# Optimization experiments

Measured on AMD Instinct MI355X. Metric: run time of the kernel, lower is better.

The kernel has to match this reference:

```python
import jax, jax.numpy as jnp
import numpy as np


def _shift_kernels():
    # [4,1,3,3] OIHW: left, right, up, down shift-difference kernels (as in torch module)
    kl = [[0, 0, 0], [-1, 1, 0], [0, 0, 0]]
    kr = [[0, 0, 0], [0, 1, -1], [0, 0, 0]]
    ku = [[0, -1, 0], [0, 1, 0], [0, 0, 0]]
    kd = [[0, 0, 0], [0, 1, 0], [0, -1, 0]]
    return jnp.asarray(np.stack([kl, kr, ku, kd])[:, None], dtype=jnp.float32)


def _avgpool4(x):
    # x: [B,1,H,W] -> [B,1,H//4,W//4], non-overlapping 4x4 mean (nn.AvgPool2d(4))
    b, c, h, w = x.shape
    return x.reshape(b, c, h // 4, 4, w // 4, 4).mean(axis=(3, 5))


def setup_inputs() -> dict:
    key = jax.random.key(0)
    k1, k2 = jax.random.split(key)
    org = jax.random.uniform(k1, (32, 3, 512, 512), dtype=jnp.float32)
    enhance = jax.random.uniform(k2, (32, 3, 512, 512), dtype=jnp.float32)
    return {"org": org, "enhance": enhance}


def reference(org, enhance):
    org_pool = _avgpool4(jnp.mean(org, axis=1, keepdims=True))
    enh_pool = _avgpool4(jnp.mean(enhance, axis=1, keepdims=True))
    # conv is linear, so D_org_k - D_enh_k == conv(org_pool - enh_pool, k).
    diff = org_pool - enh_pool  # [B,1,h,w]
    d = jax.lax.conv_general_dilated(
        diff, _shift_kernels(), window_strides=(1, 1),
        padding=((1, 1), (1, 1)),
        dimension_numbers=("NCHW", "OIHW", "NCHW"))  # [B,4,h,w]
    # torch: mean(D_left + D_right + D_up + D_down) over [B,1,h,w]
    return jnp.mean(jnp.sum(d * d, axis=1))
```

## Files before the change

kernel.cpp:

```cpp
#include <hip/hip_runtime.h>

#define NB 32
#define NC 3
#define NH 512
#define NW 512
#define PH 128
#define PW 128
#define NPOOL  (NB * PH * PW)
#define NPLANE (NB * NC)
#define PLANE_ELEMS (PH * PW)
#define NITEMS (NPLANE * PLANE_ELEMS)
#define NBLK_A 1024
#define ITEMS_A 6
#define STRIDE_A (NBLK_A * 256)
#define NBLK_RED (NPOOL / 256)

typedef float vf4 __attribute__((ext_vector_type(4)));

__device__ __forceinline__ int item_base(int item) {
    return ((item >> 14) << 16) + (((item >> 7) & 127) << 9) + (item & 127);
}

__global__ __launch_bounds__(256) void stageA_pool_kernel(
    const vf4* __restrict__ o4, const vf4* __restrict__ e4,
    float* __restrict__ partial)
{
    int item = blockIdx.x * 256 + threadIdx.x;

    int base = item_base(item);
    vf4 oc0 = __builtin_nontemporal_load(o4 + base);
    vf4 oc1 = __builtin_nontemporal_load(o4 + base + 128);
    vf4 oc2 = __builtin_nontemporal_load(o4 + base + 256);
    vf4 oc3 = __builtin_nontemporal_load(o4 + base + 384);
    vf4 ec0 = __builtin_nontemporal_load(e4 + base);
    vf4 ec1 = __builtin_nontemporal_load(e4 + base + 128);
    vf4 ec2 = __builtin_nontemporal_load(e4 + base + 256);
    vf4 ec3 = __builtin_nontemporal_load(e4 + base + 384);

#pragma unroll
    for (int it = 0; it < ITEMS_A; ++it) {
        vf4 on0, on1, on2, on3, en0, en1, en2, en3;
        if (it < ITEMS_A - 1) {
            int nbase = item_base(item + STRIDE_A);
            on0 = __builtin_nontemporal_load(o4 + nbase);
            on1 = __builtin_nontemporal_load(o4 + nbase + 128);
            on2 = __builtin_nontemporal_load(o4 + nbase + 256);
            on3 = __builtin_nontemporal_load(o4 + nbase + 384);
            en0 = __builtin_nontemporal_load(e4 + nbase);
            en1 = __builtin_nontemporal_load(e4 + nbase + 128);
            en2 = __builtin_nontemporal_load(e4 + nbase + 256);
            en3 = __builtin_nontemporal_load(e4 + nbase + 384);
        }

        vf4 d = ((oc0 - ec0) + (oc1 - ec1)) + ((oc2 - ec2) + (oc3 - ec3));
        float v = (d.x + d.y) + (d.z + d.w);
        partial[item] = v * (1.0f / 48.0f);

        if (it < ITEMS_A - 1) {
            oc0 = on0; oc1 = on1; oc2 = on2; oc3 = on3;
            ec0 = en0; ec1 = en1; ec2 = en2; ec3 = en3;
            item += STRIDE_A;
        }
    }
}

__global__ __launch_bounds__(256) void spa_reduce_kernel(
    const float* __restrict__ partial, float* __restrict__ partials_out)
{
    int idx = blockIdx.x * blockDim.x + threadIdx.x;
    int pw = idx & (PW - 1);
    int ph = (idx >> 7) & (PH - 1);
    int b  = idx >> 14;

    const float* p0 = partial + (b * 3 + 0) * PLANE_ELEMS;
    const float* p1 = partial + (b * 3 + 1) * PLANE_ELEMS;
    const float* p2 = partial + (b * 3 + 2) * PLANE_ELEMS;

    #define POOLED(y, x) (p0[(y) * PW + (x)] + p1[(y) * PW + (x)] + p2[(y) * PW + (x)])
    float c = POOLED(ph, pw);
    float l = (pw > 0)      ? POOLED(ph, pw - 1) : 0.f;
    float r = (pw < PW - 1) ? POOLED(ph, pw + 1) : 0.f;
    float u = (ph > 0)      ? POOLED(ph - 1, pw) : 0.f;
    float d = (ph < PH - 1) ? POOLED(ph + 1, pw) : 0.f;
    #undef POOLED

    float dl = c - l, dr = c - r, du = c - u, dd = c - d;
    float s = (dl * dl + dr * dr) + (du * du + dd * dd);

#pragma unroll
    for (int off = 32; off > 0; off >>= 1)
        s += __shfl_down(s, off, 64);

    __shared__ float smem[4];
    int lane = threadIdx.x & 63;
    int wid  = threadIdx.x >> 6;
    if (lane == 0) smem[wid] = s;
    __syncthreads();
    if (threadIdx.x == 0)
        partials_out[blockIdx.x] = (smem[0] + smem[1]) + (smem[2] + smem[3]);
}

__global__ __launch_bounds__(256) void final_reduce_kernel(
    const float* __restrict__ partials, float* __restrict__ out)
{
    float s = 0.f;
#pragma unroll
    for (int i = 0; i < NBLK_RED / 256; ++i)
        s += partials[i * 256 + threadIdx.x];

#pragma unroll
    for (int off = 32; off > 0; off >>= 1)
        s += __shfl_down(s, off, 64);

    __shared__ float smem[4];
    int lane = threadIdx.x & 63;
    int wid  = threadIdx.x >> 6;
    if (lane == 0) smem[wid] = s;
    __syncthreads();
    if (threadIdx.x == 0)
        out[0] = ((smem[0] + smem[1]) + (smem[2] + smem[3])) * (1.0f / (float)NPOOL);
}

extern "C" void kernel_launch(void* const* d_in, const int* in_sizes, int n_in,
                              void* d_out, int out_size, void* d_ws, size_t ws_size,
                              hipStream_t stream) {
    const vf4* o4 = (const vf4*)d_in[0];
    const vf4* e4 = (const vf4*)d_in[1];
    float* out = (float*)d_out;
    float* partial      = (float*)d_ws;
    float* blockpartial = (float*)d_ws + NITEMS;

    stageA_pool_kernel<<<NBLK_A, 256, 0, stream>>>(o4, e4, partial);
    spa_reduce_kernel<<<NBLK_RED, 256, 0, stream>>>(partial, blockpartial);
    final_reduce_kernel<<<1, 256, 0, stream>>>(blockpartial, out);
}
```

Before: 197.6 us.

## Fuse channel sum into pooling, replace final reduce kernel with atomics

The pooling kernel now reads all three channels per output pixel (12 vector loads each of org and enhance) and writes a single pooled plane per batch, instead of per-channel partials. This cuts the intermediate buffer to a third and simplifies the stencil kernel's reads. The final reduction kernel is removed in favour of one atomicAdd per block into the output, which the first kernel zeroes. This saves a launch but makes float summation order nondeterministic, and drops the software pipelining of the old loop in favour of more loads in flight per thread.

```diff
diff --git a/kernel.cpp b/kernel.cpp
--- a/kernel.cpp
+++ b/kernel.cpp
@@ -1,90 +1,59 @@
 #include <hip/hip_runtime.h>
 
 #define NB 32
-#define NC 3
-#define NH 512
-#define NW 512
 #define PH 128
 #define PW 128
 #define NPOOL  (NB * PH * PW)
-#define NPLANE (NB * NC)
-#define PLANE_ELEMS (PH * PW)
-#define NITEMS (NPLANE * PLANE_ELEMS)
-#define NBLK_A 1024
-#define ITEMS_A 6
-#define STRIDE_A (NBLK_A * 256)
-#define NBLK_RED (NPOOL / 256)
+#define NBLK   (NPOOL / 256)
+#define INV48  (1.0f / 48.0f)
 
 typedef float vf4 __attribute__((ext_vector_type(4)));
 
-__device__ __forceinline__ int item_base(int item) {
-    return ((item >> 14) << 16) + (((item >> 7) & 127) << 9) + (item & 127);
-}
+__global__ __launch_bounds__(256) void pool_fused_kernel(
+    const vf4* __restrict__ o4, const vf4* __restrict__ e4,
+    float* __restrict__ pooled, float* __restrict__ out)
+{
+    if (blockIdx.x == 0 && threadIdx.x == 0) out[0] = 0.f;
 
-__global__ __launch_bounds__(256) void stageA_pool_kernel(
-    const vf4* __restrict__ o4, const vf4* __restrict__ e4,
-    float* __restrict__ partial)
-{
-    int item = blockIdx.x * 256 + threadIdx.x;
+    int idx = blockIdx.x * 256 + threadIdx.x;
+    int x = idx & (PW - 1);
+    int y = (idx >> 7) & (PH - 1);
+    int b = idx >> 14;
 
-    int base = item_base(item);
-    vf4 oc0 = __builtin_nontemporal_load(o4 + base);
-    vf4 oc1 = __builtin_nontemporal_load(o4 + base + 128);
-    vf4 oc2 = __builtin_nontemporal_load(o4 + base + 256);
-    vf4 oc3 = __builtin_nontemporal_load(o4 + base + 384);
-    vf4 ec0 = __builtin_nontemporal_load(e4 + base);
-    vf4 ec1 = __builtin_nontemporal_load(e4 + base + 128);
-    vf4 ec2 = __builtin_nontemporal_load(e4 + base + 256);
-    vf4 ec3 = __builtin_nontemporal_load(e4 + base + 384);
+    int rbase = ((b * 3) * 512 + (y << 2)) * 128 + x;
 
+    vf4 ov[12], ev[12];
 #pragma unroll
-    for (int it = 0; it < ITEMS_A; ++it) {
-        vf4 on0, on1, on2, on3, en0, en1, en2, en3;
-        if (it < ITEMS_A - 1) {
-            int nbase = item_base(item + STRIDE_A);
-            on0 = __builtin_nontemporal_load(o4 + nbase);
-            on1 = __builtin_nontemporal_load(o4 + nbase + 128);
-            on2 = __builtin_nontemporal_load(o4 + nbase + 256);
-            on3 = __builtin_nontemporal_load(o4 + nbase + 384);
-            en0 = __builtin_nontemporal_load(e4 + nbase);
-            en1 = __builtin_nontemporal_load(e4 + nbase + 128);
-            en2 = __builtin_nontemporal_load(e4 + nbase + 256);
-            en3 = __builtin_nontemporal_load(e4 + nbase + 384);
-        }
+    for (int i = 0; i < 12; ++i) {
+        int c = i >> 2, dy = i & 3;
+        int a = rbase + (c * 512 + dy) * 128;
+        ov[i] = __builtin_nontemporal_load(o4 + a);
+        ev[i] = __builtin_nontemporal_load(e4 + a);
+    }
 
-        vf4 d = ((oc0 - ec0) + (oc1 - ec1)) + ((oc2 - ec2) + (oc3 - ec3));
-        float v = (d.x + d.y) + (d.z + d.w);
-        partial[item] = v * (1.0f / 48.0f);
+    vf4 d = {0.f, 0.f, 0.f, 0.f};
+#pragma unroll
+    for (int i = 0; i < 12; ++i)
+        d += ov[i] - ev[i];
 
-        if (it < ITEMS_A - 1) {
-            oc0 = on0; oc1 = on1; oc2 = on2; oc3 = on3;
-            ec0 = en0; ec1 = en1; ec2 = en2; ec3 = en3;
-            item += STRIDE_A;
-        }
-    }
+    pooled[idx] = ((d.x + d.y) + (d.z + d.w)) * INV48;
 }
 
 __global__ __launch_bounds__(256) void spa_reduce_kernel(
-    const float* __restrict__ partial, float* __restrict__ partials_out)
+    const float* __restrict__ pooled, float* __restrict__ out)
 {
-    int idx = blockIdx.x * blockDim.x + threadIdx.x;
-    int pw = idx & (PW - 1);
-    int ph = (idx >> 7) & (PH - 1);
-    int b  = idx >> 14;
+    int idx = blockIdx.x * 256 + threadIdx.x;
+    int x = idx & (PW - 1);
+    int y = (idx >> 7) & (PH - 1);
+    const float* p = pooled + (idx >> 14) * (PH * PW);
 
-    const float* p0 = partial + (b * 3 + 0) * PLANE_ELEMS;
-    const float* p1 = partial + (b * 3 + 1) * PLANE_ELEMS;
-    const float* p2 = partial + (b * 3 + 2) * PLANE_ELEMS;
+    float c  = p[y * PW + x];
+    float l  = (x > 0)      ? p[y * PW + x - 1] : 0.f;
+    float r  = (x < PW - 1) ? p[y * PW + x + 1] : 0.f;
+    float u  = (y > 0)      ? p[(y - 1) * PW + x] : 0.f;
+    float dn = (y < PH - 1) ? p[(y + 1) * PW + x] : 0.f;
 
-    #define POOLED(y, x) (p0[(y) * PW + (x)] + p1[(y) * PW + (x)] + p2[(y) * PW + (x)])
-    float c = POOLED(ph, pw);
-    float l = (pw > 0)      ? POOLED(ph, pw - 1) : 0.f;
-    float r = (pw < PW - 1) ? POOLED(ph, pw + 1) : 0.f;
-    float u = (ph > 0)      ? POOLED(ph - 1, pw) : 0.f;
-    float d = (ph < PH - 1) ? POOLED(ph + 1, pw) : 0.f;
-    #undef POOLED
-
-    float dl = c - l, dr = c - r, du = c - u, dd = c - d;
+    float dl = c - l, dr = c - r, du = c - u, dd = c - dn;
     float s = (dl * dl + dr * dr) + (du * du + dd * dd);
 
 #pragma unroll
@@ -97,28 +66,8 @@
     if (lane == 0) smem[wid] = s;
     __syncthreads();
     if (threadIdx.x == 0)
-        partials_out[blockIdx.x] = (smem[0] + smem[1]) + (smem[2] + smem[3]);
-}
-
-__global__ __launch_bounds__(256) void final_reduce_kernel(
-    const float* __restrict__ partials, float* __restrict__ out)
-{
-    float s = 0.f;
-#pragma unroll
-    for (int i = 0; i < NBLK_RED / 256; ++i)
-        s += partials[i * 256 + threadIdx.x];
-
-#pragma unroll
-    for (int off = 32; off > 0; off >>= 1)
-        s += __shfl_down(s, off, 64);
-
-    __shared__ float smem[4];
-    int lane = threadIdx.x & 63;
-    int wid  = threadIdx.x >> 6;
-    if (lane == 0) smem[wid] = s;
-    __syncthreads();
-    if (threadIdx.x == 0)
-        out[0] = ((smem[0] + smem[1]) + (smem[2] + smem[3])) * (1.0f / (float)NPOOL);
+        atomicAdd(out, ((smem[0] + smem[1]) + (smem[2] + smem[3]))
+                           * (1.0f / (float)NPOOL));
 }
 
 extern "C" void kernel_launch(void* const* d_in, const int* in_sizes, int n_in,
@@ -126,11 +75,9 @@
                               hipStream_t stream) {
     const vf4* o4 = (const vf4*)d_in[0];
     const vf4* e4 = (const vf4*)d_in[1];
-    float* out = (float*)d_out;
-    float* partial      = (float*)d_ws;
-    float* blockpartial = (float*)d_ws + NITEMS;
+    float* out    = (float*)d_out;
+    float* pooled = (float*)d_ws;
 
-    stageA_pool_kernel<<<NBLK_A, 256, 0, stream>>>(o4, e4, partial);
-    spa_reduce_kernel<<<NBLK_RED, 256, 0, stream>>>(partial, blockpartial);
-    final_reduce_kernel<<<1, 256, 0, stream>>>(blockpartial, out);
+    pool_fused_kernel<<<NBLK, 256, 0, stream>>>(o4, e4, pooled, out);
+    spa_reduce_kernel<<<NBLK, 256, 0, stream>>>(pooled, out);
 }
```

Result: slower. 219.4 us (+11.0%).
